# Optimization experiments

Hardware: AMD Instinct MI355X
Metric: run time of the kernel (lower is better)

Reference implementation:

```python
import jax, jax.numpy as jnp
import numpy as np
from jax import lax

B, C, H, W = 16, 64, 256, 256
EPS = 1e-5


def conv2d(x, w, b, pad):
    # x: [B,Cin,H,W], w: [Cout,Cin,kh,kw]
    out = lax.conv_general_dilated(x, w, (1, 1), [(pad, pad), (pad, pad)],
                                   dimension_numbers=("NCHW", "OIHW", "NCHW"))
    return out + b[None, :, None, None]


def setup_inputs() -> dict:
    key = jax.random.key(0)
    ks = jax.random.split(key, 12)
    s = 0.05
    return {
        "x": jax.random.normal(ks[0], (B, C, H, W), jnp.float32),
        "conv_w": jax.random.normal(ks[1], (C, C, 3, 3), jnp.float32) * s,
        "conv_b": jax.random.normal(ks[2], (C,), jnp.float32) * s,
        "bn_gamma": jnp.ones((C,), jnp.float32),
        "bn_beta": jnp.zeros((C,), jnp.float32),
        "bn_mean": jax.random.normal(ks[3], (C,), jnp.float32) * s,
        "bn_var": jax.random.uniform(ks[4], (C,), jnp.float32, 0.5, 1.5),
        "attn_w": jax.random.normal(ks[5], (1, C, 1, 1), jnp.float32) * s,
        "attn_b": jax.random.normal(ks[6], (1,), jnp.float32) * s,
        "dir1_w": jax.random.normal(ks[7], (8, C, 1, 1), jnp.float32) * s,
        "dir1_b": jax.random.normal(ks[8], (8,), jnp.float32) * s,
        "dir2_w": jax.random.normal(ks[9], (1, 8, 1, 1), jnp.float32) * s,
        "dir2_b": jax.random.normal(ks[10], (1,), jnp.float32) * s,
    }


def reference(x, conv_w, conv_b, bn_gamma, bn_beta, bn_mean, bn_var,
              attn_w, attn_b, dir1_w, dir1_b, dir2_w, dir2_b):
    # conv -> BN (eval) -> ReLU
    feat = conv2d(x, conv_w, conv_b, pad=1)
    feat = (feat - bn_mean[None, :, None, None]) * (
        bn_gamma[None, :, None, None] * lax.rsqrt(bn_var + EPS)[None, :, None, None]
    ) + bn_beta[None, :, None, None]
    feat = jax.nn.relu(feat)

    # direction branch: global avg pool -> 1x1 conv -> relu -> 1x1 conv -> sigmoid
    pooled = jnp.mean(x, axis=(2, 3))                      # [B,C]
    h1 = jax.nn.relu(pooled @ dir1_w[:, :, 0, 0].T + dir1_b)  # [B,8]
    direction = jax.nn.sigmoid(h1 @ dir2_w[:, :, 0, 0].T + dir2_b)  # [B,1]
    direction = direction[:, :, None, None]                # [B,1,1,1]

    # attention map [B,1,H,W]
    att = jnp.einsum("bchw,oc->bohw", feat, attn_w[:, :, 0, 0]) + attn_b[None, :, None, None]

    # trapezoid mask: per-row weight depending on direction > 0.5
    j = jnp.arange(H, dtype=x.dtype) / H                   # [H]
    w_up = 0.5 + 0.5 * j
    w_dn = 1.0 - 0.5 * j
    cond = direction[:, 0, 0, 0] > 0.5                     # [B]
    mask = jnp.where(cond[:, None], w_up[None, :], w_dn[None, :])  # [B,H]
    mask = mask[:, None, :, None]                          # [B,1,H,1]

    att = jax.nn.sigmoid(att * mask)
    return x * att, direction
```

## Files before the change

### kernel.cpp

```cpp
#include <hip/hip_runtime.h>

typedef __attribute__((ext_vector_type(8))) short  s8v;
typedef __attribute__((ext_vector_type(4))) float  f4v;
typedef __attribute__((ext_vector_type(4))) unsigned short u4v;

#define XH 256
#define XW 256
#define XC 64
#define PLANE 65536
#define PCW 66

__device__ __forceinline__ unsigned short f2bf(float f){
  unsigned int u = __builtin_bit_cast(unsigned int, f);
  return (unsigned short)((u + 0x7FFFu + ((u >> 16) & 1u)) >> 16);
}
__device__ __forceinline__ float bf2f(unsigned short h){
  unsigned int u = ((unsigned int)h) << 16;
  return __builtin_bit_cast(float, u);
}

__global__ __launch_bounds__(256) void pool_k(const float* __restrict__ x,
                                              float* __restrict__ pooled){
  int plane = blockIdx.x, t = threadIdx.x;
  const f4v* p = (const f4v*)(x + (size_t)plane * PLANE);
  float s = 0.f;
  #pragma unroll 8
  for(int it = 0; it < 64; ++it){
    f4v v = p[t + (it << 8)];
    s += v[0] + v[1] + v[2] + v[3];
  }
  #pragma unroll
  for(int m = 32; m >= 1; m >>= 1) s += __shfl_xor(s, m);
  __shared__ float ps[4];
  if((t & 63) == 0) ps[t >> 6] = s;
  __syncthreads();
  if(t == 0) pooled[plane] = (ps[0] + ps[1] + ps[2] + ps[3]) * (1.f / 65536.f);
}

__global__ __launch_bounds__(256) void prep_k(const float* __restrict__ convw,
    const float* __restrict__ convb, const float* __restrict__ gamma,
    const float* __restrict__ beta,  const float* __restrict__ mean,
    const float* __restrict__ var,   const float* __restrict__ d1w,
    const float* __restrict__ d1b,   const float* __restrict__ d2w,
    const float* __restrict__ d2b,   const float* __restrict__ pooled,
    float* __restrict__ dirv, float* __restrict__ bias2,
    unsigned short* __restrict__ pk, float* __restrict__ outdir){
  int blk = blockIdx.x, t = threadIdx.x;
  if(blk == 0){
    if(t < 16){
      float logit = d2b[0];
      for(int o = 0; o < 8; ++o){
        float a = d1b[o];
        for(int c = 0; c < 64; ++c) a = fmaf(pooled[t * 64 + c], d1w[o * 64 + c], a);
        logit = fmaf(fmaxf(a, 0.f), d2w[o], logit);
      }
      float dv = 1.f / (1.f + __expf(-logit));
      dirv[t] = dv;
      outdir[t] = dv;
    } else if(t >= 64 && t < 128){
      int oc = t - 64;
      float sc = gamma[oc] * rsqrtf(var[oc] + 1e-5f);
      bias2[oc] = (convb[oc] - mean[oc]) * sc + beta[oc];
    }
  } else {
    int idx = ((blk - 1) << 8) + t;
    int j = idx & 7, g = (idx >> 3) & 3, n = (idx >> 5) & 63, s = idx >> 11;
    int c = ((s & 1) << 5) + (g << 3) + j, tap = s >> 1;
    float sc = gamma[n] * rsqrtf(var[n] + 1e-5f);
    pk[idx] = f2bf(convw[(n * 64 + c) * 9 + tap] * sc);
  }
}

__global__ __launch_bounds__(256, 3) void main_k(const float* __restrict__ x,
    const float* __restrict__ attnw, const float* __restrict__ attnb,
    const float* __restrict__ dirv,  const float* __restrict__ bias2,
    const unsigned short* __restrict__ pk, float* __restrict__ out){
  __shared__ __align__(16) char lds[6 * PCW * 128 + 4 * 64 * 4];
  float* att_s = (float*)(lds + 6 * PCW * 128);

  const int bid = blockIdx.x;
  const int bs  = ((bid & 7) << 9) | (bid >> 3);
  const int wblk = bs & 3, hblk = (bs >> 2) & 63, b = bs >> 8;
  const int w0 = wblk << 6, h0 = hblk << 2;
  const int t = threadIdx.x, lane = t & 63, wv = t >> 6;
  const int lm = lane & 15, lg = lane >> 4;
  const size_t bbase = (size_t)b * XC * PLANE;

  #pragma unroll 1
  for(int it = 0; it < 7; ++it){
    int task = t + (it << 8);
    if(task < 1728){
      unsigned ut = (unsigned)task;
      int chunk = ut % 18u; unsigned rem = ut / 18u;
      int hh = rem % 6u;    int cgrp = rem / 6u;
      int hhg = h0 - 1 + hh;
      int wcg = w0 - 4 + (chunk << 2);
      f4v v0 = {0,0,0,0}, v1 = {0,0,0,0}, v2 = {0,0,0,0}, v3 = {0,0,0,0};
      if(hhg >= 0 && hhg < XH && wcg >= 0 && wcg + 3 < XW){
        const float* bp = x + bbase + (size_t)(cgrp << 2) * PLANE + (size_t)hhg * XW + wcg;
        v0 = *(const f4v*)bp;
        v1 = *(const f4v*)(bp + PLANE);
        v2 = *(const f4v*)(bp + 2 * PLANE);
        v3 = *(const f4v*)(bp + 3 * PLANE);
      }
      #pragma unroll
      for(int e = 0; e < 4; ++e){
        int pc = (chunk << 2) - 3 + e;
        if(pc >= 0 && pc < PCW){
          int pix = hh * PCW + pc;
          int bo = pix * 128 + ((cgrp << 3) ^ ((pix & 7) << 4));
          u4v pv; pv[0] = f2bf(v0[e]); pv[1] = f2bf(v1[e]);
                  pv[2] = f2bf(v2[e]); pv[3] = f2bf(v3[e]);
          *(u4v*)(lds + bo) = pv;
        }
      }
    }
  }
  __syncthreads();

  f4v acc[4][4];
  #pragma unroll
  for(int i = 0; i < 4; ++i)
    #pragma unroll
    for(int j = 0; j < 4; ++j) acc[i][j] = (f4v){0.f, 0.f, 0.f, 0.f};

  const char* pkl = (const char*)pk + lm * 64 + (lg << 4);
  const int pixb = (wv + 1) * PCW + lm + 1;
  const int cbg  = lg << 4;

  s8v bA[4], bB[4];
  #pragma unroll
  for(int jn = 0; jn < 4; ++jn) bA[jn] = *(const s8v*)(pkl + (jn << 10));

#define ALOAD(AFR, D, CB) { \
    _Pragma("unroll") \
    for(int i = 0; i < 4; ++i){ int pix = pixb + (i << 4) + (D); \
      AFR[i] = *(const s8v*)(lds + pix * 128 + ((CB) ^ ((pix & 7) << 4))); } }
#define BLOAD(BUF, S) { \
    _Pragma("unroll") \
    for(int jn = 0; jn < 4; ++jn) BUF[jn] = *(const s8v*)(pkl + ((S) << 12) + (jn << 10)); }
#define MF(AFR, BUF) { \
    _Pragma("unroll") \
    for(int i = 0; i < 4; ++i){ _Pragma("unroll") for(int j = 0; j < 4; ++j) \
      acc[i][j] = __builtin_amdgcn_mfma_f32_16x16x32_bf16(AFR[i], BUF[j], acc[i][j], 0, 0, 0); } }

  #pragma unroll 1
  for(int p = 0; p < 9; ++p){
    const int dh = p / 3 - 1, dw = p % 3 - 1;
    const int d = dh * PCW + dw;
    s8v afr[4];
    ALOAD(afr, d, cbg);
    BLOAD(bB, 2 * p + 1);
    MF(afr, bA);
    ALOAD(afr, d, cbg + 64);
    if(p < 8) BLOAD(bA, 2 * p + 2);
    MF(afr, bB);
  }

  float aw[4], bz[4];
  #pragma unroll
  for(int j = 0; j < 4; ++j){ aw[j] = attnw[(j << 4) + lm]; bz[j] = bias2[(j << 4) + lm]; }
  #pragma unroll
  for(int i = 0; i < 4; ++i){
    #pragma unroll
    for(int r = 0; r < 4; ++r){
      float lsum = 0.f;
      #pragma unroll
      for(int j = 0; j < 4; ++j)
        lsum = fmaf(aw[j], fmaxf(acc[i][j][r] + bz[j], 0.f), lsum);
      lsum += __shfl_xor(lsum, 8);
      lsum += __shfl_xor(lsum, 4);
      lsum += __shfl_xor(lsum, 2);
      lsum += __shfl_xor(lsum, 1);
      if(lm == (i << 2) + r) att_s[(wv << 6) + (i << 4) + (lg << 2) + r] = lsum;
    }
  }
  __syncthreads();

  const int col = lane, row = wv;
  const float dir = dirv[b];
  const int h = h0 + row;
  const float jf = (float)h * (1.f / 256.f);
  const float maskv = (dir > 0.5f) ? (0.5f + 0.5f * jf) : (1.f - 0.5f * jf);
  const float att = att_s[(row << 6) + col] + attnb[0];
  const float sg = 1.f / (1.f + __expf(-att * maskv));
  const int pix = (row + 1) * PCW + (col + 1);
  const char* xr = lds + pix * 128;
  const int swz = (pix & 7) << 4;
  float* op = out + bbase + (size_t)h * XW + w0 + col;
  #pragma unroll
  for(int k = 0; k < 8; ++k){
    s8v v = *(const s8v*)(xr + ((k << 4) ^ swz));
    #pragma unroll
    for(int e = 0; e < 8; ++e){
      op[(size_t)((k << 3) + e) * PLANE] = bf2f((unsigned short)v[e]) * sg;
    }
  }
#undef ALOAD
#undef BLOAD
#undef MF
}

extern "C" void kernel_launch(void* const* d_in, const int* in_sizes, int n_in,
                              void* d_out, int out_size, void* d_ws, size_t ws_size,
                              hipStream_t stream){
  const float* x     = (const float*)d_in[0];
  const float* convw = (const float*)d_in[1];
  const float* convb = (const float*)d_in[2];
  const float* gamma = (const float*)d_in[3];
  const float* beta  = (const float*)d_in[4];
  const float* mean  = (const float*)d_in[5];
  const float* var   = (const float*)d_in[6];
  const float* attnw = (const float*)d_in[7];
  const float* attnb = (const float*)d_in[8];
  const float* d1w   = (const float*)d_in[9];
  const float* d1b   = (const float*)d_in[10];
  const float* d2w   = (const float*)d_in[11];
  const float* d2b   = (const float*)d_in[12];
  float* out = (float*)d_out;
  char*  ws  = (char*)d_ws;
  float* pooled = (float*)ws;
  float* dirv   = (float*)(ws + 4096);
  float* bias2  = (float*)(ws + 4160);
  unsigned short* pk = (unsigned short*)(ws + 4416);
  float* outdir = out + (size_t)16 * 64 * 256 * 256;

  pool_k<<<1024, 256, 0, stream>>>(x, pooled);
  prep_k<<<145, 256, 0, stream>>>(convw, convb, gamma, beta, mean, var,
                                  d1w, d1b, d2w, d2b, pooled, dirv, bias2, pk, outdir);
  main_k<<<4096, 256, 0, stream>>>(x, attnw, attnb, dirv, bias2, pk, out);
}
```

Measured before the change: 630.5 us.

## Triple-buffer weight loads, fully unroll MFMA loop, remap staging tasks, parallelize prep

Fully unrolls the 18-step conv MFMA loop and keeps three weight-fragment buffers in flight, issuing the first loads before the input staging phase so global latency overlaps the LDS fill. It wraps the MFMAs in s_setprio, remaps staging task indices so the channel group is the fastest-varying index, and switches f2bf to the library bf16 conversion. The direction MLP in prep_k is split across 128 threads using shared memory. Together these aim to hide weight-load latency and cut per-thread serial work, at the cost of more vector registers, which may strain occupancy under the 3-blocks-per-CU launch bound.

```diff
diff --git a/kernel.cpp b/kernel.cpp
--- a/kernel.cpp
+++ b/kernel.cpp
@@ -1,4 +1,5 @@
 #include <hip/hip_runtime.h>
+#include <hip/hip_bf16.h>
 
 typedef __attribute__((ext_vector_type(8))) short  s8v;
 typedef __attribute__((ext_vector_type(4))) float  f4v;
@@ -11,8 +12,8 @@
 #define PCW 66
 
 __device__ __forceinline__ unsigned short f2bf(float f){
-  unsigned int u = __builtin_bit_cast(unsigned int, f);
-  return (unsigned short)((u + 0x7FFFu + ((u >> 16) & 1u)) >> 16);
+  __hip_bfloat16 h = __float2bfloat16(f);
+  return __builtin_bit_cast(unsigned short, h);
 }
 __device__ __forceinline__ float bf2f(unsigned short h){
   unsigned int u = ((unsigned int)h) << 16;
@@ -47,20 +48,26 @@
     unsigned short* __restrict__ pk, float* __restrict__ outdir){
   int blk = blockIdx.x, t = threadIdx.x;
   if(blk == 0){
+    __shared__ float h1s[16][8];
+    if(t < 128){
+      int b = t >> 3, o = t & 7;
+      float a = d1b[o];
+      #pragma unroll 8
+      for(int c = 0; c < 64; ++c) a = fmaf(pooled[b * 64 + c], d1w[o * 64 + c], a);
+      h1s[b][o] = fmaxf(a, 0.f);
+    } else if(t >= 128 && t < 192){
+      int oc = t - 128;
+      float sc = gamma[oc] * rsqrtf(var[oc] + 1e-5f);
+      bias2[oc] = (convb[oc] - mean[oc]) * sc + beta[oc];
+    }
+    __syncthreads();
     if(t < 16){
       float logit = d2b[0];
-      for(int o = 0; o < 8; ++o){
-        float a = d1b[o];
-        for(int c = 0; c < 64; ++c) a = fmaf(pooled[t * 64 + c], d1w[o * 64 + c], a);
-        logit = fmaf(fmaxf(a, 0.f), d2w[o], logit);
-      }
+      #pragma unroll
+      for(int o = 0; o < 8; ++o) logit = fmaf(h1s[t][o], d2w[o], logit);
       float dv = 1.f / (1.f + __expf(-logit));
       dirv[t] = dv;
       outdir[t] = dv;
-    } else if(t >= 64 && t < 128){
-      int oc = t - 64;
-      float sc = gamma[oc] * rsqrtf(var[oc] + 1e-5f);
-      bias2[oc] = (convb[oc] - mean[oc]) * sc + beta[oc];
     }
   } else {
     int idx = ((blk - 1) << 8) + t;
@@ -86,13 +93,22 @@
   const int lm = lane & 15, lg = lane >> 4;
   const size_t bbase = (size_t)b * XC * PLANE;
 
+  const char* pkl = (const char*)pk + lm * 64 + (lg << 4);
+
+#define BLOAD(BUF, S) { \
+    _Pragma("unroll") \
+    for(int jn = 0; jn < 4; ++jn) BUF[jn] = *(const s8v*)(pkl + ((S) << 12) + (jn << 10)); }
+
+  s8v bb0[4], bb1[4], bb2[4];
+  BLOAD(bb0, 0); BLOAD(bb1, 1); BLOAD(bb2, 2);
+
   #pragma unroll 1
   for(int it = 0; it < 7; ++it){
     int task = t + (it << 8);
     if(task < 1728){
-      unsigned ut = (unsigned)task;
-      int chunk = ut % 18u; unsigned rem = ut / 18u;
-      int hh = rem % 6u;    int cgrp = rem / 6u;
+      int cgrp = task & 15;
+      unsigned rem = (unsigned)task >> 4;
+      int hh = rem % 6u;  int chunk = rem / 6u;
       int hhg = h0 - 1 + hh;
       int wcg = w0 - 4 + (chunk << 2);
       f4v v0 = {0,0,0,0}, v1 = {0,0,0,0}, v2 = {0,0,0,0}, v3 = {0,0,0,0};
@@ -124,38 +140,32 @@
     #pragma unroll
     for(int j = 0; j < 4; ++j) acc[i][j] = (f4v){0.f, 0.f, 0.f, 0.f};
 
-  const char* pkl = (const char*)pk + lm * 64 + (lg << 4);
   const int pixb = (wv + 1) * PCW + lm + 1;
   const int cbg  = lg << 4;
-
-  s8v bA[4], bB[4];
-  #pragma unroll
-  for(int jn = 0; jn < 4; ++jn) bA[jn] = *(const s8v*)(pkl + (jn << 10));
 
 #define ALOAD(AFR, D, CB) { \
     _Pragma("unroll") \
     for(int i = 0; i < 4; ++i){ int pix = pixb + (i << 4) + (D); \
       AFR[i] = *(const s8v*)(lds + pix * 128 + ((CB) ^ ((pix & 7) << 4))); } }
-#define BLOAD(BUF, S) { \
-    _Pragma("unroll") \
-    for(int jn = 0; jn < 4; ++jn) BUF[jn] = *(const s8v*)(pkl + ((S) << 12) + (jn << 10)); }
 #define MF(AFR, BUF) { \
     _Pragma("unroll") \
     for(int i = 0; i < 4; ++i){ _Pragma("unroll") for(int j = 0; j < 4; ++j) \
       acc[i][j] = __builtin_amdgcn_mfma_f32_16x16x32_bf16(AFR[i], BUF[j], acc[i][j], 0, 0, 0); } }
-
-  #pragma unroll 1
-  for(int p = 0; p < 9; ++p){
-    const int dh = p / 3 - 1, dw = p % 3 - 1;
-    const int d = dh * PCW + dw;
-    s8v afr[4];
-    ALOAD(afr, d, cbg);
-    BLOAD(bB, 2 * p + 1);
-    MF(afr, bA);
-    ALOAD(afr, d, cbg + 64);
-    if(p < 8) BLOAD(bA, 2 * p + 2);
-    MF(afr, bB);
-  }
+#define STEPX(S, BUF) { \
+    s8v afr[4]; \
+    const int dd = (((S) >> 1) / 3 - 1) * PCW + (((S) >> 1) % 3 - 1); \
+    ALOAD(afr, dd, (((S) & 1) ? cbg + 64 : cbg)); \
+    __builtin_amdgcn_s_setprio(1); \
+    MF(afr, BUF); \
+    __builtin_amdgcn_s_setprio(0); \
+    if((S) + 3 < 18) BLOAD(BUF, (S) + 3); }
+
+  STEPX(0,  bb0) STEPX(1,  bb1) STEPX(2,  bb2)
+  STEPX(3,  bb0) STEPX(4,  bb1) STEPX(5,  bb2)
+  STEPX(6,  bb0) STEPX(7,  bb1) STEPX(8,  bb2)
+  STEPX(9,  bb0) STEPX(10, bb1) STEPX(11, bb2)
+  STEPX(12, bb0) STEPX(13, bb1) STEPX(14, bb2)
+  STEPX(15, bb0) STEPX(16, bb1) STEPX(17, bb2)
 
   float aw[4], bz[4];
   #pragma unroll
@@ -199,6 +209,7 @@
 #undef ALOAD
 #undef BLOAD
 #undef MF
+#undef STEPX
 }
 
 extern "C" void kernel_launch(void* const* d_in, const int* in_sizes, int n_in,
```

Measured after the change: 631.8 us. No clear change (+0.2%).
